# Optimization experiments

Hardware: AMD Instinct MI355X
Metric: run time of the kernel (lower is better)

Reference implementation:

```python
import jax, jax.numpy as jnp
import numpy as np
import math

D_MODEL = 1024
NUM_HEADS = 16
D_K = D_MODEL // NUM_HEADS  # 64
B, S = 4, 2048


def setup_inputs() -> dict:
    key = jax.random.key(0)
    ks = jax.random.split(key, 9)
    sc = 1.0 / math.sqrt(D_MODEL)
    return {
        "x": jax.random.normal(ks[0], (B, S, D_MODEL), jnp.float32),
        "Wq": jax.random.normal(ks[1], (D_MODEL, D_MODEL), jnp.float32) * sc,
        "bq": jax.random.normal(ks[2], (D_MODEL,), jnp.float32) * 0.01,
        "Wk": jax.random.normal(ks[3], (D_MODEL, D_MODEL), jnp.float32) * sc,
        "bk": jax.random.normal(ks[4], (D_MODEL,), jnp.float32) * 0.01,
        "Wv": jax.random.normal(ks[5], (D_MODEL, D_MODEL), jnp.float32) * sc,
        "bv": jax.random.normal(ks[6], (D_MODEL,), jnp.float32) * 0.01,
        "Wo": jax.random.normal(ks[7], (D_MODEL, D_MODEL), jnp.float32) * sc,
        "bo": jax.random.normal(ks[8], (D_MODEL,), jnp.float32) * 0.01,
    }


def reference(x, Wq, bq, Wk, bk, Wv, bv, Wo, bo):
    b, s, d = x.shape
    # Linear projections (torch Linear: x @ W.T + b)
    Q = x @ Wq.T + bq
    K = x @ Wk.T + bk
    V = x @ Wv.T + bv
    # [b, s, h*d_k] -> [b, h, s, d_k]
    split = lambda t: t.reshape(b, s, NUM_HEADS, D_K).transpose(0, 2, 1, 3)
    Q, K, V = split(Q), split(K), split(V)
    # Causal mask: query i can attend to keys j <= i
    seq = jnp.arange(s)
    causal = seq[:, None] >= seq[None, :]  # [s, s]
    # Scaled dot-product attention
    scores = jnp.einsum('bhqd,bhkd->bhqk', Q, K) / math.sqrt(D_K)
    scores = jnp.where(causal, scores, -jnp.inf)
    weights = jax.nn.softmax(scores, axis=-1)
    attn = jnp.einsum('bhqk,bhkd->bhqd', weights, V)
    # [b, h, s, d_v] -> [b, s, h*d_v]
    attn = attn.transpose(0, 2, 1, 3).reshape(b, s, NUM_HEADS * D_K)
    return attn @ Wo.T + bo
```

## Files before the change

kernel.cpp:

```cpp
#include <hip/hip_runtime.h>
#include <hip/hip_bf16.h>


typedef unsigned short u16;
typedef __attribute__((ext_vector_type(4))) short short4v;
typedef __attribute__((ext_vector_type(8))) short short8;
typedef __attribute__((ext_vector_type(4))) float f32x4;

#define KDIM   1024
#define S_LEN  2048
#define NHEADS 16
#define DK     64
#define NEG_BIG (-30000.0f)
#define QSCALE 0.18033688011112043f

__device__ __forceinline__ u16 f2bf(float f) {
  unsigned u = __float_as_uint(f);
  return (u16)((u + 0x7FFFu + ((u >> 16) & 1u)) >> 16);
}
__device__ __forceinline__ void gl_lds16(const u16* g, u16* l) {
  __builtin_amdgcn_global_load_lds((const __attribute__((address_space(1))) void*)g,
                                   (__attribute__((address_space(3))) void*)l, 16, 0, 0);
}

__global__ __launch_bounds__(256) void cvt_kernel(
    const float* __restrict__ x,  const float* __restrict__ Wq,
    const float* __restrict__ Wk, const float* __restrict__ Wv,
    u16* __restrict__ xb, u16* __restrict__ wqb,
    u16* __restrict__ wkb, u16* __restrict__ wvb) {
  const int NX = 2097152, NW = 262144;
  const int total = NX + 3 * NW;
  for (int i = blockIdx.x * 256 + threadIdx.x; i < total; i += gridDim.x * 256) {
    const float* src; u16* dst; int off;
    if (i < NX)               { src = x;  dst = xb;  off = i; }
    else if (i < NX + NW)     { src = Wq; dst = wqb; off = i - NX; }
    else if (i < NX + 2 * NW) { src = Wk; dst = wkb; off = i - NX - NW; }
    else                      { src = Wv; dst = wvb; off = i - NX - 2 * NW; }
    f32x4 v = *(const f32x4*)(src + (size_t)off * 4);
    short4v o;
    o[0] = (short)f2bf(v[0]); o[1] = (short)f2bf(v[1]);
    o[2] = (short)f2bf(v[2]); o[3] = (short)f2bf(v[3]);
    *(short4v*)(dst + (size_t)off * 4) = o;
  }
}

__global__ __launch_bounds__(256) void cvt_wo(const float* __restrict__ W,
                                              u16* __restrict__ out) {
  const int i = blockIdx.x * 256 + threadIdx.x;
  f32x4 v = *(const f32x4*)(W + (size_t)i * 4);
  short4v o;
  o[0] = (short)f2bf(v[0]); o[1] = (short)f2bf(v[1]);
  o[2] = (short)f2bf(v[2]); o[3] = (short)f2bf(v[3]);
  *(short4v*)(out + (size_t)i * 4) = o;
}

__device__ __forceinline__ void gemm_body(const u16* __restrict__ A,
                                          const u16* __restrict__ B,
                                          const float* __restrict__ bias,
                                          void* __restrict__ outv, int mode) {
  __shared__ __align__(16) u16 As[128 * 32];
  __shared__ __align__(16) u16 Bs[128 * 32];
  const int tid = threadIdx.x;
  const int wave = tid >> 6, lane = tid & 63;
  const int quad = lane >> 4, l16 = lane & 15;
  const int wy = wave >> 1, wx = wave & 1;
  const int m0 = blockIdx.x * 128, n0 = blockIdx.y * 128;

  f32x4 acc[4][4];
#pragma unroll
  for (int i = 0; i < 4; i++)
#pragma unroll
    for (int j = 0; j < 4; j++) acc[i][j] = (f32x4){0.f, 0.f, 0.f, 0.f};

  const int srow = wave * 16 + (lane >> 2);
  const int scol = (lane & 3) * 8;
  const u16* gA0 = A + (size_t)(m0 + srow) * KDIM + scol;
  const u16* gA1 = gA0 + (size_t)64 * KDIM;
  const u16* gB0 = B + (size_t)(n0 + srow) * KDIM + scol;
  const u16* gB1 = gB0 + (size_t)64 * KDIM;
  u16* lA0 = &As[srow * 32 + scol];
  u16* lA1 = lA0 + 2048;
  u16* lB0 = &Bs[srow * 32 + scol];
  u16* lB1 = lB0 + 2048;

  for (int k = 0; k < KDIM; k += 32) {
    __syncthreads();
    gl_lds16(gA0 + k, lA0);
    gl_lds16(gA1 + k, lA1);
    gl_lds16(gB0 + k, lB0);
    gl_lds16(gB1 + k, lB1);
    __syncthreads();
    short8 af[4], bfr[4];
#pragma unroll
    for (int i = 0; i < 4; i++)
      af[i] = *(const short8*)&As[(wy * 64 + i * 16 + l16) * 32 + quad * 8];
#pragma unroll
    for (int j = 0; j < 4; j++)
      bfr[j] = *(const short8*)&Bs[(wx * 64 + j * 16 + l16) * 32 + quad * 8];
#pragma unroll
    for (int i = 0; i < 4; i++)
#pragma unroll
      for (int j = 0; j < 4; j++)
        acc[i][j] = __builtin_amdgcn_mfma_f32_16x16x32_bf16(af[i], bfr[j], acc[i][j], 0, 0, 0);
  }

#pragma unroll
  for (int j = 0; j < 4; j++) {
    const int col = n0 + wx * 64 + j * 16 + l16;
    const float bv = bias[col];
#pragma unroll
    for (int i = 0; i < 4; i++) {
      const int rowb = m0 + wy * 64 + i * 16 + quad * 4;
#pragma unroll
      for (int r = 0; r < 4; r++) {
        float v = acc[i][j][r] + bv;
        const int row = rowb + r;
        if (mode == 3) {
          ((float*)outv)[(size_t)row * 1024 + col] = v;
        } else {
          const int b = row >> 11, s = row & 2047;
          const int h = col >> 6, d = col & 63;
          if (mode == 0) v *= QSCALE;
          size_t idx;
          if (mode == 2) idx = (((size_t)(b * NHEADS + h)) * DK + d) * S_LEN + s;
          else           idx = (((size_t)(b * NHEADS + h)) * S_LEN + s) * DK + d;
          ((u16*)outv)[idx] = f2bf(v);
        }
      }
    }
  }
}

__global__ __launch_bounds__(256) void qkv_gemm(
    const u16* __restrict__ xb,
    const u16* __restrict__ wqb, const float* __restrict__ bq,
    const u16* __restrict__ wkb, const float* __restrict__ bk,
    const u16* __restrict__ wvb, const float* __restrict__ bv,
    u16* __restrict__ qb, u16* __restrict__ kb, u16* __restrict__ vb) {
  const u16* W; const float* bias; u16* out; int mode;
  if (blockIdx.z == 0)      { W = wqb; bias = bq; out = qb; mode = 0; }
  else if (blockIdx.z == 1) { W = wkb; bias = bk; out = kb; mode = 1; }
  else                      { W = wvb; bias = bv; out = vb; mode = 2; }
  gemm_body(xb, W, bias, out, mode);
}

__global__ __launch_bounds__(256) void out_gemm(const u16* __restrict__ A,
                                                const u16* __restrict__ wob,
                                                const float* __restrict__ bo,
                                                float* __restrict__ out) {
  gemm_body(A, wob, bo, out, 3);
}

__global__ __launch_bounds__(256) void attn_kernel(const u16* __restrict__ Qb,
                                                   const u16* __restrict__ Kb,
                                                   const u16* __restrict__ Vb,
                                                   u16* __restrict__ Ob) {
  __shared__ __align__(16) u16 Ks[64 * 72];
  __shared__ __align__(16) u16 Vt[64 * 72];
  __shared__ __align__(16) u16 Ps[4 * 16 * 72];
  const int bh = blockIdx.x;
  const int qt = (int)gridDim.y - 1 - (int)blockIdx.y;
  const int tid = threadIdx.x, wave = tid >> 6, lane = tid & 63;
  const int quad = lane >> 4, l16 = lane & 15;
  const u16* Qh = Qb + (size_t)bh * S_LEN * DK;
  const u16* Kh = Kb + (size_t)bh * S_LEN * DK;
  const u16* Vh = Vb + (size_t)bh * S_LEN * DK;

  const int qrow = qt * 64 + wave * 16 + l16;
  const short8 qf0 = *(const short8*)&Qh[(size_t)qrow * DK + quad * 8];
  const short8 qf1 = *(const short8*)&Qh[(size_t)qrow * DK + 32 + quad * 8];

  short8 ones;
#pragma unroll
  for (int i = 0; i < 8; i++) ones[i] = (short)0x3F80;

  f32x4 o[4];
#pragma unroll
  for (int j = 0; j < 4; j++) o[j] = (f32x4){0.f, 0.f, 0.f, 0.f};
  f32x4 l_acc = (f32x4){0.f, 0.f, 0.f, 0.f};

  const int srow = tid >> 2;
  const int scol = (tid & 3) * 16;
  const int qrow_acc = qt * 64 + wave * 16 + quad * 4;
  u16* Pw = &Ps[wave * 16 * 72];

  for (int t = 0; t <= qt; ++t) {
    const int kbase = t * 64;
    __syncthreads();
    const u16* kp = &Kh[(size_t)(kbase + srow) * DK + scol];
    short8 k0 = *(const short8*)kp;
    short8 k1 = *(const short8*)(kp + 8);
    const u16* vp = &Vh[(size_t)srow * S_LEN + kbase + scol];
    short8 v0 = *(const short8*)vp;
    short8 v1 = *(const short8*)(vp + 8);
    *(short8*)&Ks[srow * 72 + scol]     = k0;
    *(short8*)&Ks[srow * 72 + scol + 8] = k1;
    *(short8*)&Vt[srow * 72 + scol]     = v0;
    *(short8*)&Vt[srow * 72 + scol + 8] = v1;
    __syncthreads();

    f32x4 sc[4];
#pragma unroll
    for (int j = 0; j < 4; j++) {
      short8 b0 = *(const short8*)&Ks[(j * 16 + l16) * 72 + quad * 8];
      short8 b1 = *(const short8*)&Ks[(j * 16 + l16) * 72 + 32 + quad * 8];
      f32x4 c = (f32x4){0.f, 0.f, 0.f, 0.f};
      c = __builtin_amdgcn_mfma_f32_16x16x32_bf16(qf0, b0, c, 0, 0, 0);
      c = __builtin_amdgcn_mfma_f32_16x16x32_bf16(qf1, b1, c, 0, 0, 0);
      sc[j] = c;
    }

    if (t == qt) {
#pragma unroll
      for (int j = 0; j < 4; j++) {
        const int key = kbase + j * 16 + l16;
#pragma unroll
        for (int r = 0; r < 4; r++)
          sc[j][r] = (key > qrow_acc + r) ? NEG_BIG : sc[j][r];
      }
    }

#pragma unroll
    for (int j = 0; j < 4; j++)
#pragma unroll
      for (int r = 0; r < 4; r++)
        Pw[(quad * 4 + r) * 72 + j * 16 + l16] = f2bf(exp2f(sc[j][r]));
    const short8 pa0 = *(const short8*)&Pw[l16 * 72 + quad * 8];
    const short8 pa1 = *(const short8*)&Pw[l16 * 72 + 32 + quad * 8];
    l_acc = __builtin_amdgcn_mfma_f32_16x16x32_bf16(pa0, ones, l_acc, 0, 0, 0);
    l_acc = __builtin_amdgcn_mfma_f32_16x16x32_bf16(pa1, ones, l_acc, 0, 0, 0);
#pragma unroll
    for (int j = 0; j < 4; j++) {
      short8 vb0 = *(const short8*)&Vt[(j * 16 + l16) * 72 + quad * 8];
      short8 vb1 = *(const short8*)&Vt[(j * 16 + l16) * 72 + 32 + quad * 8];
      o[j] = __builtin_amdgcn_mfma_f32_16x16x32_bf16(pa0, vb0, o[j], 0, 0, 0);
      o[j] = __builtin_amdgcn_mfma_f32_16x16x32_bf16(pa1, vb1, o[j], 0, 0, 0);
    }
  }

  const int b = bh >> 4, h = bh & 15;
  float inv[4];
#pragma unroll
  for (int r = 0; r < 4; r++) inv[r] = __builtin_amdgcn_rcpf(l_acc[r]);
#pragma unroll
  for (int j = 0; j < 4; j++) {
    const int col = h * DK + j * 16 + l16;
#pragma unroll
    for (int r = 0; r < 4; r++) {
      const int s = qrow_acc + r;
      Ob[((size_t)b * S_LEN + s) * 1024 + col] = f2bf(o[j][r] * inv[r]);
    }
  }
}

extern "C" void kernel_launch(void* const* d_in, const int* in_sizes, int n_in,
                              void* d_out, int out_size, void* d_ws, size_t ws_size,
                              hipStream_t stream) {
  const float* x  = (const float*)d_in[0];
  const float* Wq = (const float*)d_in[1];
  const float* bq = (const float*)d_in[2];
  const float* Wk = (const float*)d_in[3];
  const float* bk = (const float*)d_in[4];
  const float* Wv = (const float*)d_in[5];
  const float* bv = (const float*)d_in[6];
  const float* Wo = (const float*)d_in[7];
  const float* bo = (const float*)d_in[8];

  u16* outh = (u16*)d_out;
  u16* wsh  = (u16*)d_ws;
  u16* qb  = outh;
  u16* xb  = outh + (size_t)8388608;
  u16* kb  = wsh;
  u16* vb  = wsh + (size_t)8388608;
  u16* ab  = wsh + (size_t)16777216;
  u16* wqb = ab;
  u16* wkb = wqb + (size_t)1048576;
  u16* wvb = wkb + (size_t)1048576;
  u16* wob = kb;

  cvt_kernel<<<dim3(2048), 256, 0, stream>>>(x, Wq, Wk, Wv, xb, wqb, wkb, wvb);
  qkv_gemm<<<dim3(64, 8, 3), 256, 0, stream>>>(xb, wqb, bq, wkb, bk, wvb, bv, qb, kb, vb);
  attn_kernel<<<dim3(64, 32), 256, 0, stream>>>(qb, kb, vb, ab);
  cvt_wo<<<dim3(1024), 256, 0, stream>>>(Wo, wob);
  out_gemm<<<dim3(64, 8), 256, 0, stream>>>(ab, wob, bo, (float*)d_out);
}
```

Baseline: 280.4 us.

## Vectorize GEMM/attention epilogues via transposed MFMA and async LDS loads for K/V

GEMM epilogues are templated on mode and swap the MFMA operand order for Q/K/out so each lane holds four consecutive columns. This allows packed 8-byte bf16 stores and 16-byte float stores instead of scalar writes. The attention kernel now loads K/V tiles with global_load_lds directly into unpadded split LDS buffers, transposes the score MFMA so P is written packed, and uses a cheaper round-half-up bf16 conversion. Unpadded 32-wide LDS rows may introduce bank conflicts on reads, and the rounding differs slightly from round-to-nearest-even.

```diff
diff --git a/kernel.cpp b/kernel.cpp
--- a/kernel.cpp
+++ b/kernel.cpp
@@ -3,6 +3,8 @@
 
 
 typedef unsigned short u16;
+typedef unsigned int u32;
+typedef __attribute__((ext_vector_type(2))) unsigned int uint2v;
 typedef __attribute__((ext_vector_type(4))) short short4v;
 typedef __attribute__((ext_vector_type(8))) short short8;
 typedef __attribute__((ext_vector_type(4))) float f32x4;
@@ -17,6 +19,11 @@
 __device__ __forceinline__ u16 f2bf(float f) {
   unsigned u = __float_as_uint(f);
   return (u16)((u + 0x7FFFu + ((u >> 16) & 1u)) >> 16);
+}
+__device__ __forceinline__ u32 pkbf(float a, float b) {
+  u32 ua = __float_as_uint(a) + 0x8000u;
+  u32 ub = __float_as_uint(b) + 0x8000u;
+  return __builtin_amdgcn_perm(ub, ua, 0x07060302u);
 }
 __device__ __forceinline__ void gl_lds16(const u16* g, u16* l) {
   __builtin_amdgcn_global_load_lds((const __attribute__((address_space(1))) void*)g,
@@ -54,10 +61,11 @@
   *(short4v*)(out + (size_t)i * 4) = o;
 }
 
+template <int MODE>
 __device__ __forceinline__ void gemm_body(const u16* __restrict__ A,
                                           const u16* __restrict__ B,
                                           const float* __restrict__ bias,
-                                          void* __restrict__ outv, int mode) {
+                                          void* __restrict__ outv) {
   __shared__ __align__(16) u16 As[128 * 32];
   __shared__ __align__(16) u16 Bs[128 * 32];
   const int tid = threadIdx.x;
@@ -100,32 +108,57 @@
 #pragma unroll
     for (int i = 0; i < 4; i++)
 #pragma unroll
-      for (int j = 0; j < 4; j++)
-        acc[i][j] = __builtin_amdgcn_mfma_f32_16x16x32_bf16(af[i], bfr[j], acc[i][j], 0, 0, 0);
-  }
-
-#pragma unroll
-  for (int j = 0; j < 4; j++) {
-    const int col = n0 + wx * 64 + j * 16 + l16;
-    const float bv = bias[col];
-#pragma unroll
-    for (int i = 0; i < 4; i++) {
-      const int rowb = m0 + wy * 64 + i * 16 + quad * 4;
-#pragma unroll
-      for (int r = 0; r < 4; r++) {
-        float v = acc[i][j][r] + bv;
-        const int row = rowb + r;
-        if (mode == 3) {
-          ((float*)outv)[(size_t)row * 1024 + col] = v;
-        } else {
-          const int b = row >> 11, s = row & 2047;
-          const int h = col >> 6, d = col & 63;
-          if (mode == 0) v *= QSCALE;
-          size_t idx;
-          if (mode == 2) idx = (((size_t)(b * NHEADS + h)) * DK + d) * S_LEN + s;
-          else           idx = (((size_t)(b * NHEADS + h)) * S_LEN + s) * DK + d;
-          ((u16*)outv)[idx] = f2bf(v);
-        }
+      for (int j = 0; j < 4; j++) {
+        if (MODE == 2)
+          acc[i][j] = __builtin_amdgcn_mfma_f32_16x16x32_bf16(af[i], bfr[j], acc[i][j], 0, 0, 0);
+        else
+          acc[i][j] = __builtin_amdgcn_mfma_f32_16x16x32_bf16(bfr[j], af[i], acc[i][j], 0, 0, 0);
+      }
+  }
+
+  if (MODE == 0 || MODE == 1) {
+#pragma unroll
+    for (int j = 0; j < 4; j++) {
+      const int colb = n0 + wx * 64 + j * 16 + quad * 4;
+      const int h = colb >> 6, d0 = colb & 63;
+      const f32x4 bv4 = *(const f32x4*)&bias[colb];
+#pragma unroll
+      for (int i = 0; i < 4; i++) {
+        const int row = m0 + wy * 64 + i * 16 + l16;
+        const int b = row >> 11, s = row & 2047;
+        float v0 = acc[i][j][0] + bv4[0], v1 = acc[i][j][1] + bv4[1];
+        float v2 = acc[i][j][2] + bv4[2], v3 = acc[i][j][3] + bv4[3];
+        if (MODE == 0) { v0 *= QSCALE; v1 *= QSCALE; v2 *= QSCALE; v3 *= QSCALE; }
+        uint2v pk = {pkbf(v0, v1), pkbf(v2, v3)};
+        *(uint2v*)&((u16*)outv)[(((size_t)(b * NHEADS + h)) * S_LEN + s) * DK + d0] = pk;
+      }
+    }
+  } else if (MODE == 2) {
+#pragma unroll
+    for (int j = 0; j < 4; j++) {
+      const int col = n0 + wx * 64 + j * 16 + l16;
+      const int h = col >> 6, d = col & 63;
+      const float bvs = bias[col];
+#pragma unroll
+      for (int i = 0; i < 4; i++) {
+        const int rowb = m0 + wy * 64 + i * 16 + quad * 4;
+        const int b = rowb >> 11, s0 = rowb & 2047;
+        uint2v pk = {pkbf(acc[i][j][0] + bvs, acc[i][j][1] + bvs),
+                     pkbf(acc[i][j][2] + bvs, acc[i][j][3] + bvs)};
+        *(uint2v*)&((u16*)outv)[(((size_t)(b * NHEADS + h)) * DK + d) * S_LEN + s0] = pk;
+      }
+    }
+  } else {
+#pragma unroll
+    for (int j = 0; j < 4; j++) {
+      const int colb = n0 + wx * 64 + j * 16 + quad * 4;
+      const f32x4 bv4 = *(const f32x4*)&bias[colb];
+#pragma unroll
+      for (int i = 0; i < 4; i++) {
+        const int row = m0 + wy * 64 + i * 16 + l16;
+        f32x4 v = {acc[i][j][0] + bv4[0], acc[i][j][1] + bv4[1],
+                   acc[i][j][2] + bv4[2], acc[i][j][3] + bv4[3]};
+        *(f32x4*)&((float*)outv)[(size_t)row * 1024 + colb] = v;
       }
     }
   }
@@ -137,26 +170,26 @@
     const u16* __restrict__ wkb, const float* __restrict__ bk,
     const u16* __restrict__ wvb, const float* __restrict__ bv,
     u16* __restrict__ qb, u16* __restrict__ kb, u16* __restrict__ vb) {
-  const u16* W; const float* bias; u16* out; int mode;
-  if (blockIdx.z == 0)      { W = wqb; bias = bq; out = qb; mode = 0; }
-  else if (blockIdx.z == 1) { W = wkb; bias = bk; out = kb; mode = 1; }
-  else                      { W = wvb; bias = bv; out = vb; mode = 2; }
-  gemm_body(xb, W, bias, out, mode);
+  if (blockIdx.z == 0)      gemm_body<0>(xb, wqb, bq, qb);
+  else if (blockIdx.z == 1) gemm_body<1>(xb, wkb, bk, kb);
+  else                      gemm_body<2>(xb, wvb, bv, vb);
 }
 
 __global__ __launch_bounds__(256) void out_gemm(const u16* __restrict__ A,
                                                 const u16* __restrict__ wob,
                                                 const float* __restrict__ bo,
                                                 float* __restrict__ out) {
-  gemm_body(A, wob, bo, out, 3);
+  gemm_body<3>(A, wob, bo, out);
 }
 
 __global__ __launch_bounds__(256) void attn_kernel(const u16* __restrict__ Qb,
                                                    const u16* __restrict__ Kb,
                                                    const u16* __restrict__ Vb,
                                                    u16* __restrict__ Ob) {
-  __shared__ __align__(16) u16 Ks[64 * 72];
-  __shared__ __align__(16) u16 Vt[64 * 72];
+  __shared__ __align__(16) u16 Ks0[64 * 32];
+  __shared__ __align__(16) u16 Ks1[64 * 32];
+  __shared__ __align__(16) u16 Vt0[64 * 32];
+  __shared__ __align__(16) u16 Vt1[64 * 32];
   __shared__ __align__(16) u16 Ps[4 * 16 * 72];
   const int bh = blockIdx.x;
   const int qt = (int)gridDim.y - 1 - (int)blockIdx.y;
@@ -179,62 +212,64 @@
   for (int j = 0; j < 4; j++) o[j] = (f32x4){0.f, 0.f, 0.f, 0.f};
   f32x4 l_acc = (f32x4){0.f, 0.f, 0.f, 0.f};
 
-  const int srow = tid >> 2;
-  const int scol = (tid & 3) * 16;
+  const int sr = lane >> 2, sc = lane & 3;
+  u16* dK0 = &Ks0[wave * 512 + lane * 8];
+  u16* dK1 = &Ks1[wave * 512 + lane * 8];
+  u16* dV0 = &Vt0[wave * 512 + lane * 8];
+  u16* dV1 = &Vt1[wave * 512 + lane * 8];
+  const u16* gK = Kh + (size_t)(wave * 16 + sr) * DK + sc * 8;
+  const u16* gV = Vh + (size_t)(wave * 16 + sr) * S_LEN + sc * 8;
+
   const int qrow_acc = qt * 64 + wave * 16 + quad * 4;
   u16* Pw = &Ps[wave * 16 * 72];
 
   for (int t = 0; t <= qt; ++t) {
     const int kbase = t * 64;
     __syncthreads();
-    const u16* kp = &Kh[(size_t)(kbase + srow) * DK + scol];
-    short8 k0 = *(const short8*)kp;
-    short8 k1 = *(const short8*)(kp + 8);
-    const u16* vp = &Vh[(size_t)srow * S_LEN + kbase + scol];
-    short8 v0 = *(const short8*)vp;
-    short8 v1 = *(const short8*)(vp + 8);
-    *(short8*)&Ks[srow * 72 + scol]     = k0;
-    *(short8*)&Ks[srow * 72 + scol + 8] = k1;
-    *(short8*)&Vt[srow * 72 + scol]     = v0;
-    *(short8*)&Vt[srow * 72 + scol + 8] = v1;
+    gl_lds16(gK + (size_t)kbase * DK, dK0);
+    gl_lds16(gK + (size_t)kbase * DK + 32, dK1);
+    gl_lds16(gV + kbase, dV0);
+    gl_lds16(gV + kbase + 32, dV1);
     __syncthreads();
 
-    f32x4 sc[4];
-#pragma unroll
-    for (int j = 0; j < 4; j++) {
-      short8 b0 = *(const short8*)&Ks[(j * 16 + l16) * 72 + quad * 8];
-      short8 b1 = *(const short8*)&Ks[(j * 16 + l16) * 72 + 32 + quad * 8];
+    f32x4 st[4];
+#pragma unroll
+    for (int j = 0; j < 4; j++) {
+      short8 ka0 = *(const short8*)&Ks0[(j * 16 + l16) * 32 + quad * 8];
+      short8 ka1 = *(const short8*)&Ks1[(j * 16 + l16) * 32 + quad * 8];
       f32x4 c = (f32x4){0.f, 0.f, 0.f, 0.f};
-      c = __builtin_amdgcn_mfma_f32_16x16x32_bf16(qf0, b0, c, 0, 0, 0);
-      c = __builtin_amdgcn_mfma_f32_16x16x32_bf16(qf1, b1, c, 0, 0, 0);
-      sc[j] = c;
+      c = __builtin_amdgcn_mfma_f32_16x16x32_bf16(ka0, qf0, c, 0, 0, 0);
+      c = __builtin_amdgcn_mfma_f32_16x16x32_bf16(ka1, qf1, c, 0, 0, 0);
+      st[j] = c;
     }
 
     if (t == qt) {
 #pragma unroll
       for (int j = 0; j < 4; j++) {
-        const int key = kbase + j * 16 + l16;
+        const int keyb = kbase + j * 16 + quad * 4;
 #pragma unroll
         for (int r = 0; r < 4; r++)
-          sc[j][r] = (key > qrow_acc + r) ? NEG_BIG : sc[j][r];
-      }
-    }
-
-#pragma unroll
-    for (int j = 0; j < 4; j++)
-#pragma unroll
-      for (int r = 0; r < 4; r++)
-        Pw[(quad * 4 + r) * 72 + j * 16 + l16] = f2bf(exp2f(sc[j][r]));
+          st[j][r] = (keyb + r > qrow) ? NEG_BIG : st[j][r];
+      }
+    }
+
+#pragma unroll
+    for (int j = 0; j < 4; j++) {
+      float e0 = exp2f(st[j][0]), e1 = exp2f(st[j][1]);
+      float e2 = exp2f(st[j][2]), e3 = exp2f(st[j][3]);
+      uint2v pk = {pkbf(e0, e1), pkbf(e2, e3)};
+      *(uint2v*)&Pw[l16 * 72 + j * 16 + quad * 4] = pk;
+    }
     const short8 pa0 = *(const short8*)&Pw[l16 * 72 + quad * 8];
     const short8 pa1 = *(const short8*)&Pw[l16 * 72 + 32 + quad * 8];
     l_acc = __builtin_amdgcn_mfma_f32_16x16x32_bf16(pa0, ones, l_acc, 0, 0, 0);
     l_acc = __builtin_amdgcn_mfma_f32_16x16x32_bf16(pa1, ones, l_acc, 0, 0, 0);
 #pragma unroll
-    for (int j = 0; j < 4; j++) {
-      short8 vb0 = *(const short8*)&Vt[(j * 16 + l16) * 72 + quad * 8];
-      short8 vb1 = *(const short8*)&Vt[(j * 16 + l16) * 72 + 32 + quad * 8];
-      o[j] = __builtin_amdgcn_mfma_f32_16x16x32_bf16(pa0, vb0, o[j], 0, 0, 0);
-      o[j] = __builtin_amdgcn_mfma_f32_16x16x32_bf16(pa1, vb1, o[j], 0, 0, 0);
+    for (int jd = 0; jd < 4; jd++) {
+      short8 vb0 = *(const short8*)&Vt0[(jd * 16 + l16) * 32 + quad * 8];
+      short8 vb1 = *(const short8*)&Vt1[(jd * 16 + l16) * 32 + quad * 8];
+      o[jd] = __builtin_amdgcn_mfma_f32_16x16x32_bf16(pa0, vb0, o[jd], 0, 0, 0);
+      o[jd] = __builtin_amdgcn_mfma_f32_16x16x32_bf16(pa1, vb1, o[jd], 0, 0, 0);
     }
   }
 
@@ -243,12 +278,14 @@
 #pragma unroll
   for (int r = 0; r < 4; r++) inv[r] = __builtin_amdgcn_rcpf(l_acc[r]);
 #pragma unroll
-  for (int j = 0; j < 4; j++) {
-    const int col = h * DK + j * 16 + l16;
+  for (int jd = 0; jd < 4; jd++) {
+    const int col = h * DK + jd * 16 + l16;
 #pragma unroll
     for (int r = 0; r < 4; r++) {
       const int s = qrow_acc + r;
-      Ob[((size_t)b * S_LEN + s) * 1024 + col] = f2bf(o[j][r] * inv[r]);
+      float v = o[jd][r] * inv[r];
+      unsigned u = __float_as_uint(v) + 0x8000u;
+      Ob[((size_t)b * S_LEN + s) * 1024 + col] = (u16)(u >> 16);
     }
   }
 }
```

New measurement: 275.1 us. Within noise of the previous version (-1.9%).
